# Kernel optimization log

Hardware: AMD Instinct MI355X
Metric: run time of the kernel (lower is better)

## Reference

```python
import jax, jax.numpy as jnp
import numpy as np

D = 128            # actual_dim
DM = 2 * D         # d_model = 256
DI = 2 * DM        # support-encoder inner dim = 512
H = 2 * DM         # LSTMCell hidden = 512
NUM_SYMBOLS = 200000
KNN_K = 10
PROCESS_STEPS = 4
BQ, BS, NN = 4096, 128, 64


def setup_inputs() -> dict:
    key = jax.random.key(0)
    ks = jax.random.split(key, 20)
    ri = lambda k, shape, hi: jax.random.randint(k, shape, 0, hi)
    rn = lambda k, shape, s=0.05: jax.random.normal(k, shape, jnp.float32) * s
    emb = rn(ks[0], (NUM_SYMBOLS + 1, D), 0.1).at[NUM_SYMBOLS].set(0.0)  # padding row
    return {
        "query": ri(ks[1], (BQ, 2), NUM_SYMBOLS),
        "support": ri(ks[2], (BS, 2), NUM_SYMBOLS),
        "q_l_conn": ri(ks[3], (BQ, NN, 2), NUM_SYMBOLS),
        "q_l_deg": ri(ks[4], (BQ,), NN),
        "q_r_conn": ri(ks[5], (BQ, NN, 2), NUM_SYMBOLS),
        "q_r_deg": ri(ks[6], (BQ,), NN),
        "s_l_conn": ri(ks[7], (BS, NN, 2), NUM_SYMBOLS),
        "s_l_deg": ri(ks[8], (BS,), NN),
        "s_r_conn": ri(ks[9], (BS, NN, 2), NUM_SYMBOLS),
        "s_r_deg": ri(ks[10], (BS,), NN),
        "emb": emb,
        "gcn_W": rn(ks[11], (D, 2 * D)),
        "gcn_wb": jnp.zeros((D,), jnp.float32),
        "gcn_b": jnp.zeros((D,), jnp.float32),
        "se_w1": rn(ks[12], (DI, DM)),
        "se_b1": jnp.zeros((DI,), jnp.float32),
        "se_w2": rn(ks[13], (DM, DI)),
        "se_b2": jnp.zeros((DM,), jnp.float32),
        "ln_g": jnp.ones((DM,), jnp.float32),
        "ln_b": jnp.zeros((DM,), jnp.float32),
        "W_ih": rn(ks[14], (4 * H, DM)),
        "W_hh": rn(ks[15], (4 * H, H)),
        "b_ih": jnp.zeros((4 * H,), jnp.float32),
        "b_hh": jnp.zeros((4 * H,), jnp.float32),
    }


def _cos(a, b, eps=1e-8):
    num = jnp.sum(a * b, -1)
    den = jnp.maximum(jnp.linalg.norm(a, axis=-1), eps) * jnp.maximum(jnp.linalg.norm(b, axis=-1), eps)
    return num / den


def _neighbor_encoder(emb, gcn_W, gcn_wb, gcn_b, conn, ent_ids):
    rel = emb[conn[..., 0]]                     # [B,N,D]
    ent = emb[conn[..., 1]]                     # [B,N,D]
    center = emb[ent_ids][:, None, :]           # [B,1,D]
    sim = _cos(center, ent)                     # [B,N]
    _, idx = jax.lax.top_k(sim, KNN_K)          # [B,K]
    rel_k = jnp.take_along_axis(rel, idx[..., None], axis=1)
    ent_k = jnp.take_along_axis(ent, idx[..., None], axis=1)
    cat = jnp.concatenate([rel_k, ent_k], -1)   # [B,K,2D]
    h = jnp.einsum('bkf,df->bkd', cat, gcn_W) + gcn_wb + gcn_b
    return jnp.tanh(h.mean(axis=1))             # [B,D]


def _support_encoder(x, w1, b1, w2, b2, g, b):
    # residual FFN + LayerNorm (GMatching SupportEncoder), dropout off (eval)
    out = jax.nn.relu(x @ w1.T + b1) @ w2.T + b2
    y = out + x
    mu = y.mean(-1, keepdims=True)
    var = ((y - mu) ** 2).mean(-1, keepdims=True)
    return (y - mu) / jnp.sqrt(var + 1e-5) * g + b


def _query_encoder(support, query, W_ih, W_hh, b_ih, b_hh):
    # GMatching attentive LSTM process block. support: [1,DM], query: [B,DM]
    B = query.shape[0]
    h_r = jnp.zeros((B, H), query.dtype)
    c = jnp.zeros((B, H), query.dtype)
    h = query
    for _ in range(PROCESS_STEPS):
        gates = query @ W_ih.T + b_ih + h_r @ W_hh.T + b_hh
        i, f, g_, o = jnp.split(gates, 4, axis=-1)  # torch LSTMCell gate order
        c = jax.nn.sigmoid(f) * c + jax.nn.sigmoid(i) * jnp.tanh(g_)
        h_new = jax.nn.sigmoid(o) * jnp.tanh(c)     # [B,H]
        h = query + h_new[:, :DM]                   # [B,DM]
        attn = jax.nn.softmax(h @ support.T, axis=1)  # [B,1]
        r = attn @ support                          # [B,DM]
        h_r = jnp.concatenate([h, r], axis=1)       # [B,H]
    return h


def reference(query, support, q_l_conn, q_l_deg, q_r_conn, q_r_deg,
              s_l_conn, s_l_deg, s_r_conn, s_r_deg,
              emb, gcn_W, gcn_wb, gcn_b,
              se_w1, se_b1, se_w2, se_b2, ln_g, ln_b,
              W_ih, W_hh, b_ih, b_hh):
    ne = lambda conn, ids: _neighbor_encoder(emb, gcn_W, gcn_wb, gcn_b, conn, ids)
    q_nb = jnp.concatenate([ne(q_l_conn, query[:, 0]), ne(q_r_conn, query[:, 1])], -1)    # [BQ,DM]
    s_nb = jnp.concatenate([ne(s_l_conn, support[:, 0]), ne(s_r_conn, support[:, 1])], -1)  # [BS,DM]
    se = lambda x: _support_encoder(x, se_w1, se_b1, se_w2, se_b2, ln_g, ln_b)
    support_g = se(s_nb).mean(axis=0, keepdims=True)  # [1,DM]
    query_g = se(q_nb)                                # [BQ,DM]
    qf = _query_encoder(support_g, query_g, W_ih, W_hh, b_ih, b_hh)
    l2 = lambda x: x / jnp.maximum(jnp.linalg.norm(x, axis=-1, keepdims=True), 1e-12)
    return (l2(qf) @ l2(support_g).T).squeeze(-1)     # [BQ]
```

## Files before the change

### kernel.cpp

```cpp
#include <hip/hip_runtime.h>
#include <hip/hip_bf16.h>

#define D   128
#define DM  256
#define DI  512
#define HH  512
#define KNN 10
#define NN  64
#define BQ  4096
#define BS  128
#define BM2 (BQ + BS)
#define G2  1024
#define GK  256
#define NSYM 200000

__device__ __forceinline__ float sigmoidf_(float x) {
    return 1.f / (1.f + __expf(-x));
}
__device__ __forceinline__ float tanh_fast(float x) {
    x = fminf(fmaxf(x, -20.f), 20.f);
    float e = __expf(2.f * x);
    return (e - 1.f) / (e + 1.f);
}
__device__ __forceinline__ ushort f2bf(float x) {
    union { float f; unsigned u; } v; v.f = x;
    unsigned r = (v.u + 0x7fffu + ((v.u >> 16) & 1u)) >> 16;
    return (ushort)r;
}

typedef __bf16  bf16x8  __attribute__((ext_vector_type(8)));
typedef float   floatx4 __attribute__((ext_vector_type(4)));

__global__ __launch_bounds__(256) void prep_kernel(
    const float* __restrict__ W_ih, const float* __restrict__ W_hh,
    const float* __restrict__ b_ih, const float* __restrict__ b_hh,
    const float* __restrict__ se_w1, const float* __restrict__ se_w2,
    ushort* __restrict__ wih_bf, ushort* __restrict__ whh_bf,
    float* __restrict__ bsumP, ushort* __restrict__ w1_bf,
    ushort* __restrict__ w2_bf)
{
    int bid = blockIdx.x;
    int tid = threadIdx.x;
    if (bid < G2) {
        int n = bid;
        int bn = n >> 7, r = n & 127;
        int half = (r >> 6) & 1, j = (r >> 4) & 3, l = r & 15;
        int u = bn * 32 + half * 16 + l;
        int oldrow = j * 512 + u;
        wih_bf[n * 256 + tid] = f2bf(W_ih[(size_t)oldrow * DM + tid]);
        whh_bf[n * 256 + tid] = f2bf(W_hh[(size_t)oldrow * HH + tid]);
        if (tid == 0) bsumP[n] = b_ih[oldrow] + b_hh[oldrow];
    } else {
        int idx = (bid - G2) * 256 + tid;
        w1_bf[idx] = f2bf(se_w1[idx]);
        w2_bf[idx] = f2bf(se_w2[idx]);
    }
}

__global__ __launch_bounds__(256) void ne_kernel(
    const int* __restrict__ q_l, const int* __restrict__ q_r,
    const int* __restrict__ q_ids,
    const int* __restrict__ s_l, const int* __restrict__ s_r,
    const int* __restrict__ s_ids,
    const float* __restrict__ emb,
    float* __restrict__ catm_out)
{
    int bid = blockIdx.x;
    const int *conn_l, *conn_r, *ids;
    int row;
    if (bid < BQ * 2) { conn_l = q_l; conn_r = q_r; ids = q_ids; row = bid >> 1; }
    else { conn_l = s_l; conn_r = s_r; ids = s_ids; row = (bid - BQ * 2) >> 1; }
    int side = bid & 1;
    const int* conn = (side ? conn_r : conn_l) + (size_t)row * NN * 2;
    int cid = ids[row * 2 + side];

    __shared__ int   connb[NN * 2];
    __shared__ float sim[NN];
    __shared__ int   selr[KNN], sele[KNN];

    int tid = threadIdx.x;
    int wave = tid >> 6, lane = tid & 63;
    int grp = lane >> 4, l16 = lane & 15;

    if (tid < NN * 2) connb[tid] = conn[tid];
    const float* cp = &emb[(size_t)cid * D + l16 * 8];
    float4 c4a = *(const float4*)cp;
    float4 c4b = *(const float4*)(cp + 4);
    float cs = c4a.x * c4a.x + c4a.y * c4a.y + c4a.z * c4a.z + c4a.w * c4a.w
             + c4b.x * c4b.x + c4b.y * c4b.y + c4b.z * c4b.z + c4b.w * c4b.w;
    #pragma unroll
    for (int off = 8; off; off >>= 1) cs += __shfl_xor(cs, off);
    float cnorm = fmaxf(sqrtf(cs), 1e-8f);
    __syncthreads();

    float4 ea[4], eb[4];
    #pragma unroll
    for (int b = 0; b < 4; b++) {
        int j = wave * 16 + b * 4 + grp;
        int eid = connb[j * 2 + 1];
        const float* ep = &emb[(size_t)eid * D + l16 * 8];
        ea[b] = *(const float4*)ep;
        eb[b] = *(const float4*)(ep + 4);
    }
    #pragma unroll
    for (int b = 0; b < 4; b++) {
        int j = wave * 16 + b * 4 + grp;
        float dot = c4a.x * ea[b].x + c4a.y * ea[b].y + c4a.z * ea[b].z + c4a.w * ea[b].w
                  + c4b.x * eb[b].x + c4b.y * eb[b].y + c4b.z * eb[b].z + c4b.w * eb[b].w;
        float ee  = ea[b].x * ea[b].x + ea[b].y * ea[b].y + ea[b].z * ea[b].z + ea[b].w * ea[b].w
                  + eb[b].x * eb[b].x + eb[b].y * eb[b].y + eb[b].z * eb[b].z + eb[b].w * eb[b].w;
        #pragma unroll
        for (int off = 8; off; off >>= 1) {
            dot += __shfl_xor(dot, off);
            ee  += __shfl_xor(ee, off);
        }
        if (l16 == 0) sim[j] = dot / (cnorm * fmaxf(sqrtf(ee), 1e-8f));
    }
    __syncthreads();

    if (wave == 0) {
        float s = sim[lane];
        int id = lane;
        for (int k = 0; k < KNN; k++) {
            float bs = s; int bi = id;
            #pragma unroll
            for (int off = 32; off; off >>= 1) {
                float os = __shfl_xor(bs, off);
                int   oi = __shfl_xor(bi, off);
                if (os > bs || (os == bs && oi < bi)) { bs = os; bi = oi; }
            }
            if (lane == 0) { selr[k] = connb[bi * 2]; sele[k] = connb[bi * 2 + 1]; }
            if (id == bi) s = -__builtin_inff();
        }
    }
    __syncthreads();

    float acc = 0.f;
    if (tid < D) {
        #pragma unroll
        for (int k = 0; k < KNN; k++) acc += emb[(size_t)selr[k] * D + tid];
    } else {
        int d = tid - D;
        #pragma unroll
        for (int k = 0; k < KNN; k++) acc += emb[(size_t)sele[k] * D + d];
    }
    catm_out[(size_t)bid * DM + tid] = acc * (1.f / KNN);
}

#define GR 16
__global__ __launch_bounds__(256) void gcn_kernel(
    const float* __restrict__ catm, const float* __restrict__ gcn_W,
    const float* __restrict__ gcn_wb, const float* __restrict__ gcn_b,
    float* __restrict__ out, ushort* __restrict__ out_bf)
{
    __shared__ float cs[GR][DM];
    __shared__ float pp[GR][DM];
    int tid = threadIdx.x;
    int m0 = blockIdx.x * GR;
    #pragma unroll
    for (int t = 0; t < 4; t++) {
        int chunk = tid + 256 * t;
        int r = chunk >> 6, c4 = chunk & 63;
        *(float4*)&cs[r][c4 * 4] = *(const float4*)&catm[(size_t)(m0 + r) * DM + c4 * 4];
    }
    __syncthreads();

    int d = tid & 127, half = tid >> 7;
    float a[GR];
    #pragma unroll
    for (int r = 0; r < GR; r++) a[r] = 0.f;
    const float4* W4 = (const float4*)(gcn_W + (size_t)d * DM + half * D);
    for (int f4 = 0; f4 < D / 4; ++f4) {
        float4 w = W4[f4];
        #pragma unroll
        for (int r = 0; r < GR; r++) {
            const float* c = &cs[r][half * D + f4 * 4];
            a[r] += w.x * c[0] + w.y * c[1] + w.z * c[2] + w.w * c[3];
        }
    }
    #pragma unroll
    for (int r = 0; r < GR; r++) pp[r][tid] = a[r];
    __syncthreads();
    if (tid < D) {
        #pragma unroll
        for (int r = 0; r < GR; r++) {
            float h = pp[r][tid] + pp[r][tid + D] + gcn_wb[tid] + gcn_b[tid];
            float th = tanh_fast(h);
            out[(size_t)(m0 + r) * D + tid] = th;
            out_bf[(size_t)(m0 + r) * D + tid] = f2bf(th);
        }
    }
}

#define BMT 128
#define BNT 128
#define BKT 64
#define LDP (BKT + 8)

#define GEMM_CORE(AP, BP, KDIM)                                               \
    floatx4 acc[4][4];                                                        \
    _Pragma("unroll")                                                         \
    for (int i = 0; i < 4; i++)                                               \
        _Pragma("unroll")                                                     \
        for (int j = 0; j < 4; j++) acc[i][j] = (floatx4){0.f, 0.f, 0.f, 0.f};\
    for (int k0 = 0; k0 < (KDIM); k0 += BKT) {                                \
        __syncthreads();                                                      \
        _Pragma("unroll")                                                     \
        for (int t = 0; t < 4; t++) {                                         \
            int chunk = tid + 256 * t;                                        \
            int r = chunk >> 3;                                               \
            int c8 = (chunk & 7) * 8;                                         \
            *(uint4*)&As[r][c8] = *(const uint4*)&(AP)[(size_t)(bm * BMT + r) * (KDIM) + k0 + c8]; \
            *(uint4*)&Bs[r][c8] = *(const uint4*)&(BP)[(size_t)(bn * BNT + r) * (KDIM) + k0 + c8]; \
        }                                                                     \
        __syncthreads();                                                      \
        _Pragma("unroll")                                                     \
        for (int kk = 0; kk < BKT; kk += 32) {                                \
            bf16x8 af[4], bf[4];                                              \
            _Pragma("unroll")                                                 \
            for (int i = 0; i < 4; i++)                                       \
                af[i] = *(const bf16x8*)&As[wm + i * 16 + l16][kk + quad * 8];\
            _Pragma("unroll")                                                 \
            for (int j = 0; j < 4; j++)                                       \
                bf[j] = *(const bf16x8*)&Bs[wn + j * 16 + l16][kk + quad * 8];\
            _Pragma("unroll")                                                 \
            for (int i = 0; i < 4; i++)                                       \
                _Pragma("unroll")                                             \
                for (int j = 0; j < 4; j++)                                   \
                    acc[i][j] = __builtin_amdgcn_mfma_f32_16x16x32_bf16(      \
                        af[i], bf[j], acc[i][j], 0, 0, 0);                    \
        }                                                                     \
    }

#define GEMM_PRE()                                                            \
    __shared__ __align__(16) ushort As[BMT][LDP];                             \
    __shared__ __align__(16) ushort Bs[BNT][LDP];                             \
    int tid = threadIdx.x;                                                    \
    int wave = tid >> 6, lane = tid & 63;                                     \
    int quad = lane >> 4, l16 = lane & 15;                                    \
    int bm = blockIdx.x, bn = blockIdx.y;                                     \
    int wm = (wave >> 1) * 64, wn = (wave & 1) * 64;                          \
    (void)wave;

__global__ __launch_bounds__(256) void se_gemm1_kernel(
    const ushort* __restrict__ A, const ushort* __restrict__ B,
    const float* __restrict__ b1, ushort* __restrict__ Cbf)
{
    GEMM_PRE();
    GEMM_CORE(A, B, DM);
    #pragma unroll
    for (int i = 0; i < 4; i++) {
        #pragma unroll
        for (int j = 0; j < 4; j++) {
            int row = bm * BMT + wm + i * 16 + quad * 4;
            int col = bn * BNT + wn + j * 16 + l16;
            float bb = b1[col];
            #pragma unroll
            for (int rr = 0; rr < 4; rr++)
                Cbf[(size_t)(row + rr) * DI + col] = f2bf(fmaxf(acc[i][j][rr] + bb, 0.f));
        }
    }
}

__global__ __launch_bounds__(256) void se_gemm2_kernel(
    const ushort* __restrict__ A, const ushort* __restrict__ B,
    const float* __restrict__ b2, const float* __restrict__ xres,
    float* __restrict__ C)
{
    GEMM_PRE();
    GEMM_CORE(A, B, DI);
    #pragma unroll
    for (int i = 0; i < 4; i++) {
        #pragma unroll
        for (int j = 0; j < 4; j++) {
            int row = bm * BMT + wm + i * 16 + quad * 4;
            int col = bn * BNT + wn + j * 16 + l16;
            float bb = b2[col];
            #pragma unroll
            for (int rr = 0; rr < 4; rr++)
                C[(size_t)(row + rr) * DM + col] =
                    acc[i][j][rr] + bb + xres[(size_t)(row + rr) * DM + col];
        }
    }
}

#define LN_ROWS 8
__global__ __launch_bounds__(256) void ln_kernel(
    const float* __restrict__ ys, const float* __restrict__ g,
    const float* __restrict__ b, float* __restrict__ outf,
    ushort* __restrict__ outbf)
{
    int tid = threadIdx.x;
    int wave = tid >> 6, lane = tid & 63;
    int r0 = blockIdx.x * LN_ROWS;
    for (int rr = 0; rr < 2; ++rr) {
        int r = r0 + wave * 2 + rr;
        float vals[4];
        float s = 0.f;
        #pragma unroll
        for (int e = 0; e < 4; e++) {
            vals[e] = ys[(size_t)r * DM + e * 64 + lane];
            s += vals[e];
        }
        #pragma unroll
        for (int off = 32; off; off >>= 1) s += __shfl_xor(s, off);
        float mu = s * (1.f / DM);
        float v = 0.f;
        #pragma unroll
        for (int e = 0; e < 4; e++) { float dd = vals[e] - mu; v += dd * dd; }
        #pragma unroll
        for (int off = 32; off; off >>= 1) v += __shfl_xor(v, off);
        float rstd = rsqrtf(v * (1.f / DM) + 1e-5f);
        #pragma unroll
        for (int e = 0; e < 4; e++) {
            int dd = e * 64 + lane;
            float ov = (vals[e] - mu) * rstd * g[dd] + b[dd];
            outf[(size_t)r * DM + dd] = ov;
            outbf[(size_t)r * DM + dd] = f2bf(ov);
        }
    }
}

__global__ __launch_bounds__(256) void sgw_kernel(
    const float* __restrict__ ln_f, const float* __restrict__ W_hh,
    const float* __restrict__ b_ih, const float* __restrict__ b_hh,
    float* __restrict__ sg, float* __restrict__ gaddP)
{
    __shared__ float s[DM];
    int tid = threadIdx.x;
    float a = 0.f;
    for (int r = 0; r < BS; r++) a += ln_f[(size_t)(BQ + r) * DM + tid];
    a *= (1.f / BS);
    s[tid] = a;
    if (blockIdx.x == 0) sg[tid] = a;
    __syncthreads();

    int idx = blockIdx.x * 256 + tid;
    int g = idx >> 8, u = idx & 255;
    int oldrow = g * 512 + u;
    const float4* w4 = (const float4*)(W_hh + (size_t)oldrow * HH + DM);
    float acc = 0.f;
    for (int f4 = 0; f4 < DM / 4; ++f4) {
        float4 w = w4[f4];
        acc += w.x * s[f4 * 4] + w.y * s[f4 * 4 + 1] + w.z * s[f4 * 4 + 2] + w.w * s[f4 * 4 + 3];
    }
    float bs = b_ih[oldrow] + b_hh[oldrow];
    int n = (u >> 5) * 128 + ((u >> 4) & 1) * 64 + g * 16 + (u & 15);
    gaddP[n] = bs + acc;
}

__global__ __launch_bounds__(256) void lstm_gemm0_kernel(
    const ushort* __restrict__ A, const ushort* __restrict__ B,
    const float* __restrict__ bsumP, const float* __restrict__ lnf,
    float* __restrict__ P0f, float* __restrict__ Cf, ushort* __restrict__ h_out)
{
    GEMM_PRE();
    GEMM_CORE(A, B, GK);
    int u = bn * 32 + (wn ? 16 : 0) + l16;
    size_t tile = (size_t)bm * 8 + bn;
    float b4[4];
    #pragma unroll
    for (int j = 0; j < 4; j++) b4[j] = bsumP[bn * 128 + wn + j * 16 + l16];
    #pragma unroll
    for (int i = 0; i < 4; i++) {
        int row = bm * BMT + wm + i * 16 + quad * 4;
        #pragma unroll
        for (int j = 0; j < 4; j++)
            *(floatx4*)&P0f[((tile * 16 + i * 4 + j) * 256 + tid) * 4] = acc[i][j];
        floatx4 cv4;
        #pragma unroll
        for (int rr = 0; rr < 4; rr++) {
            float iv = acc[i][0][rr] + b4[0];
            float gv = acc[i][2][rr] + b4[2];
            float ov = acc[i][3][rr] + b4[3];
            float cv = sigmoidf_(iv) * tanh_fast(gv);
            cv4[rr] = cv;
            float h = lnf[(size_t)(row + rr) * DM + u] + sigmoidf_(ov) * tanh_fast(cv);
            h_out[(size_t)(row + rr) * DM + u] = f2bf(h);
        }
        *(floatx4*)&Cf[((tile * 4 + i) * 256 + tid) * 4] = cv4;
    }
}

__global__ __launch_bounds__(256) void lstm_step_kernel(
    const ushort* __restrict__ A, const ushort* __restrict__ B,
    const float* __restrict__ P0f, const float* __restrict__ gaddP,
    const float* __restrict__ lnf, float* __restrict__ Cf,
    ushort* __restrict__ h_out, float* __restrict__ hf_out, int last)
{
    GEMM_PRE();
    GEMM_CORE(A, B, GK);
    int u = bn * 32 + (wn ? 16 : 0) + l16;
    size_t tile = (size_t)bm * 8 + bn;
    float g4[4];
    #pragma unroll
    for (int j = 0; j < 4; j++) g4[j] = gaddP[bn * 128 + wn + j * 16 + l16];
    #pragma unroll
    for (int i = 0; i < 4; i++) {
        int row = bm * BMT + wm + i * 16 + quad * 4;
        floatx4 p0[4];
        #pragma unroll
        for (int j = 0; j < 4; j++)
            p0[j] = *(const floatx4*)&P0f[((tile * 16 + i * 4 + j) * 256 + tid) * 4];
        floatx4 cprev = *(const floatx4*)&Cf[((tile * 4 + i) * 256 + tid) * 4];
        floatx4 cnew;
        #pragma unroll
        for (int rr = 0; rr < 4; rr++) {
            float iv = acc[i][0][rr] + p0[0][rr] + g4[0];
            float fv = acc[i][1][rr] + p0[1][rr] + g4[1];
            float gv = acc[i][2][rr] + p0[2][rr] + g4[2];
            float ov = acc[i][3][rr] + p0[3][rr] + g4[3];
            float cv = sigmoidf_(fv) * cprev[rr] + sigmoidf_(iv) * tanh_fast(gv);
            cnew[rr] = cv;
            float h = lnf[(size_t)(row + rr) * DM + u] + sigmoidf_(ov) * tanh_fast(cv);
            if (last) hf_out[(size_t)(row + rr) * DM + u] = h;
            else      h_out[(size_t)(row + rr) * DM + u] = f2bf(h);
        }
        *(floatx4*)&Cf[((tile * 4 + i) * 256 + tid) * 4] = cnew;
    }
}

__global__ __launch_bounds__(256) void final_kernel(
    const float* __restrict__ h_ws, const float* __restrict__ sg,
    float* __restrict__ outp)
{
    __shared__ float sgs[DM];
    int tid = threadIdx.x;
    sgs[tid] = sg[tid];
    __syncthreads();
    int wave = tid >> 6, lane = tid & 63;
    float sn = 0.f;
    #pragma unroll
    for (int e = 0; e < 4; e++) { float v = sgs[e * 64 + lane]; sn += v * v; }
    #pragma unroll
    for (int off = 32; off; off >>= 1) sn += __shfl_xor(sn, off);
    float sgnorm = fmaxf(sqrtf(sn), 1e-12f);

    int row = blockIdx.x * 4 + wave;
    const float* h = h_ws + (size_t)row * DM;
    float dot = 0.f, hn = 0.f;
    #pragma unroll
    for (int e = 0; e < 4; e++) {
        float hv = h[e * 64 + lane];
        dot += hv * sgs[e * 64 + lane];
        hn += hv * hv;
    }
    #pragma unroll
    for (int off = 32; off; off >>= 1) { dot += __shfl_xor(dot, off); hn += __shfl_xor(hn, off); }
    if (lane == 0) outp[row] = dot / (fmaxf(sqrtf(hn), 1e-12f) * sgnorm);
}

extern "C" void kernel_launch(void* const* d_in, const int* in_sizes, int n_in,
                              void* d_out, int out_size, void* d_ws, size_t ws_size,
                              hipStream_t stream)
{
    const int* query    = (const int*)d_in[0];
    const int* support  = (const int*)d_in[1];
    const int* q_l_conn = (const int*)d_in[2];
    const int* q_r_conn = (const int*)d_in[4];
    const int* s_l_conn = (const int*)d_in[6];
    const int* s_r_conn = (const int*)d_in[8];
    const float* emb    = (const float*)d_in[10];
    const float* gcn_W  = (const float*)d_in[11];
    const float* gcn_wb = (const float*)d_in[12];
    const float* gcn_b  = (const float*)d_in[13];
    const float* se_w1  = (const float*)d_in[14];
    const float* se_b1  = (const float*)d_in[15];
    const float* se_w2  = (const float*)d_in[16];
    const float* se_b2  = (const float*)d_in[17];
    const float* ln_g   = (const float*)d_in[18];
    const float* ln_b   = (const float*)d_in[19];
    const float* W_ih   = (const float*)d_in[20];
    const float* W_hh   = (const float*)d_in[21];
    const float* b_ih   = (const float*)d_in[22];
    const float* b_hh   = (const float*)d_in[23];
    float* out = (float*)d_out;

    char* wsb = (char*)d_ws;
    float*  xf     = (float*)wsb;  wsb += (size_t)BM2 * DM * 4;
    ushort* xb     = (ushort*)wsb; wsb += (size_t)BM2 * DM * 2;
    ushort* t1_bf  = (ushort*)wsb; wsb += (size_t)BM2 * DI * 2;
    float*  ys     = (float*)wsb;  wsb += (size_t)BM2 * DM * 4;
    float*  ln_f   = (float*)wsb;  wsb += (size_t)BM2 * DM * 4;
    ushort* ln_bf  = (ushort*)wsb; wsb += (size_t)BM2 * DM * 2;
    float*  sg     = (float*)wsb;  wsb += DM * 4;
    float*  bsumP  = (float*)wsb;  wsb += G2 * 4;
    float*  gaddP  = (float*)wsb;  wsb += G2 * 4;
    ushort* wih_bf = (ushort*)wsb; wsb += (size_t)G2 * DM * 2;
    ushort* whh_bf = (ushort*)wsb; wsb += (size_t)G2 * DM * 2;
    ushort* w1_bf  = (ushort*)wsb; wsb += (size_t)DI * DM * 2;
    ushort* w2_bf  = (ushort*)wsb; wsb += (size_t)DM * DI * 2;
    float*  P0f    = (float*)wsb;  wsb += (size_t)BQ * G2 * 4;
    float*  Cf     = (float*)wsb;  wsb += (size_t)BQ * DM * 4;
    ushort* h_bfA  = (ushort*)wsb; wsb += (size_t)BQ * DM * 2;
    ushort* h_bfB  = (ushort*)wsb; wsb += (size_t)BQ * DM * 2;
    float*  h_f    = (float*)wsb;  wsb += (size_t)BQ * DM * 4;

    float* catm = P0f;

    prep_kernel<<<G2 + 512, 256, 0, stream>>>(
        W_ih, W_hh, b_ih, b_hh, se_w1, se_w2,
        wih_bf, whh_bf, bsumP, w1_bf, w2_bf);
    ne_kernel<<<BQ * 2 + BS * 2, 256, 0, stream>>>(
        q_l_conn, q_r_conn, query, s_l_conn, s_r_conn, support,
        emb, catm);
    gcn_kernel<<<(BM2 * 2) / GR, 256, 0, stream>>>(catm, gcn_W, gcn_wb, gcn_b,
                                                   xf, xb);
    { dim3 g1(BM2 / BMT, DI / BNT);
      se_gemm1_kernel<<<g1, 256, 0, stream>>>(xb, w1_bf, se_b1, t1_bf); }
    { dim3 g2(BM2 / BMT, DM / BNT);
      se_gemm2_kernel<<<g2, 256, 0, stream>>>(t1_bf, w2_bf, se_b2, xf, ys); }
    ln_kernel<<<BM2 / LN_ROWS, 256, 0, stream>>>(ys, ln_g, ln_b, ln_f, ln_bf);
    sgw_kernel<<<G2 / 256, 256, 0, stream>>>(ln_f, W_hh, b_ih, b_hh, sg, gaddP);

    dim3 ggrid(BQ / BMT, G2 / BNT);
    lstm_gemm0_kernel<<<ggrid, 256, 0, stream>>>(ln_bf, wih_bf, bsumP, ln_f,
                                                 P0f, Cf, h_bfA);
    lstm_step_kernel<<<ggrid, 256, 0, stream>>>(h_bfA, whh_bf, P0f, gaddP, ln_f,
                                                Cf, h_bfB, h_f, 0);
    lstm_step_kernel<<<ggrid, 256, 0, stream>>>(h_bfB, whh_bf, P0f, gaddP, ln_f,
                                                Cf, h_bfA, h_f, 0);
    lstm_step_kernel<<<ggrid, 256, 0, stream>>>(h_bfA, whh_bf, P0f, gaddP, ln_f,
                                                Cf, h_bfB, h_f, 1);
    final_kernel<<<BQ / 4, 256, 0, stream>>>(h_f, sg, out);
}
```

Before: 376.2 us.

## Fuse LSTM steps into one persistent kernel with group barriers

Replaces the four separate LSTM GEMM launches with one persistent kernel of 256 blocks. Each block keeps its input-projection result, cell state and LN residual in registers, and keeps the W_hh tile resident in LDS. The eight blocks sharing a row tile synchronise between steps through atomic counter barriers. This removes the P0f and Cf round-trips through global memory, the repeated weight reloads and the launch overhead. The cost is a spin-wait barrier that assumes all 256 blocks are co-resident, plus heavy register and LDS use at one block per CU.

```diff
diff --git a/kernel.cpp b/kernel.cpp
--- a/kernel.cpp
+++ b/kernel.cpp
@@ -37,7 +37,7 @@
     const float* __restrict__ se_w1, const float* __restrict__ se_w2,
     ushort* __restrict__ wih_bf, ushort* __restrict__ whh_bf,
     float* __restrict__ bsumP, ushort* __restrict__ w1_bf,
-    ushort* __restrict__ w2_bf)
+    ushort* __restrict__ w2_bf, int* __restrict__ lbar)
 {
     int bid = blockIdx.x;
     int tid = threadIdx.x;
@@ -50,10 +50,12 @@
         wih_bf[n * 256 + tid] = f2bf(W_ih[(size_t)oldrow * DM + tid]);
         whh_bf[n * 256 + tid] = f2bf(W_hh[(size_t)oldrow * HH + tid]);
         if (tid == 0) bsumP[n] = b_ih[oldrow] + b_hh[oldrow];
-    } else {
+    } else if (bid < G2 + 512) {
         int idx = (bid - G2) * 256 + tid;
         w1_bf[idx] = f2bf(se_w1[idx]);
         w2_bf[idx] = f2bf(se_w2[idx]);
+    } else {
+        if (tid < 128) lbar[tid] = 0;
     }
 }
 
@@ -349,74 +351,152 @@
     gaddP[n] = bs + acc;
 }
 
-__global__ __launch_bounds__(256) void lstm_gemm0_kernel(
-    const ushort* __restrict__ A, const ushort* __restrict__ B,
-    const float* __restrict__ bsumP, const float* __restrict__ lnf,
-    float* __restrict__ P0f, float* __restrict__ Cf, ushort* __restrict__ h_out)
-{
-    GEMM_PRE();
-    GEMM_CORE(A, B, GK);
+#define SWZ(r, c16) (((c16) ^ ((r) & 7)) << 3)
+
+#define STAGE_TILE(DSTARR, SRCPTR, STRIDE)                                     \
+    _Pragma("unroll")                                                          \
+    for (int t = 0; t < 16; t++) {                                             \
+        int ch = t * 256 + tid;                                                \
+        int r = ch >> 5, c16 = ch & 31;                                        \
+        *(uint4*)&DSTARR[r][SWZ(r, c16)] =                                     \
+            *(const uint4*)&(SRCPTR)[(size_t)r * (STRIDE) + c16 * 8];          \
+    }
+
+#define LDS_GEMM(ACC)                                                          \
+    _Pragma("unroll")                                                          \
+    for (int kk = 0; kk < GK; kk += 32) {                                      \
+        bf16x8 af[4], bv[4];                                                   \
+        int c16 = (kk >> 3) + quad;                                            \
+        _Pragma("unroll")                                                      \
+        for (int i = 0; i < 4; i++) {                                          \
+            int rw = wm + i * 16 + l16;                                        \
+            af[i] = *(const bf16x8*)&AS[rw][SWZ(rw, c16)];                     \
+        }                                                                      \
+        _Pragma("unroll")                                                      \
+        for (int j = 0; j < 4; j++) {                                          \
+            int rw = wn + j * 16 + l16;                                        \
+            bv[j] = *(const bf16x8*)&WS[rw][SWZ(rw, c16)];                     \
+        }                                                                      \
+        _Pragma("unroll")                                                      \
+        for (int i = 0; i < 4; i++)                                            \
+            _Pragma("unroll")                                                  \
+            for (int j = 0; j < 4; j++)                                        \
+                ACC[i][j] = __builtin_amdgcn_mfma_f32_16x16x32_bf16(           \
+                    af[i], bv[j], ACC[i][j], 0, 0, 0);                         \
+    }
+
+__device__ __forceinline__ void group_barrier(int* cnt, int tid) {
+    __threadfence();
+    __syncthreads();
+    if (tid == 0) {
+        __hip_atomic_fetch_add(cnt, 1, __ATOMIC_RELEASE, __HIP_MEMORY_SCOPE_AGENT);
+        while (__hip_atomic_load(cnt, __ATOMIC_ACQUIRE, __HIP_MEMORY_SCOPE_AGENT) < 8) {}
+    }
+    __syncthreads();
+    __threadfence();
+}
+
+__global__ __launch_bounds__(256, 1) void lstm_fused_kernel(
+    const ushort* __restrict__ lnbf,
+    const ushort* __restrict__ wihP,
+    const ushort* __restrict__ whhP,
+    const float* __restrict__ bsumP,
+    const float* __restrict__ gaddP,
+    const float* __restrict__ lnf,
+    ushort* __restrict__ hA,
+    ushort* __restrict__ hB,
+    float* __restrict__ hF,
+    int* __restrict__ lbar)
+{
+    __shared__ __align__(16) ushort AS[128][256];
+    __shared__ __align__(16) ushort WS[128][256];
+
+    int tid = threadIdx.x;
+    int wave = tid >> 6, lane = tid & 63;
+    int quad = lane >> 4, l16 = lane & 15;
+    int bid = blockIdx.x;
+    int bm = bid >> 3, bn = bid & 7;
+    int wm = (wave >> 1) * 64, wn = (wave & 1) * 64;
     int u = bn * 32 + (wn ? 16 : 0) + l16;
-    size_t tile = (size_t)bm * 8 + bn;
-    float b4[4];
-    #pragma unroll
-    for (int j = 0; j < 4; j++) b4[j] = bsumP[bn * 128 + wn + j * 16 + l16];
+    int* mybar = lbar + bm * 4;
+
+    STAGE_TILE(WS, wihP + (size_t)(bn * 128) * GK, GK);
+    STAGE_TILE(AS, lnbf + (size_t)(bm * 128) * GK, GK);
+
+    float b4[4], g4[4];
+    #pragma unroll
+    for (int j = 0; j < 4; j++) {
+        b4[j] = bsumP[bn * 128 + wn + j * 16 + l16];
+        g4[j] = gaddP[bn * 128 + wn + j * 16 + l16];
+    }
+    float lnb[4][4];
     #pragma unroll
     for (int i = 0; i < 4; i++) {
-        int row = bm * BMT + wm + i * 16 + quad * 4;
-        #pragma unroll
-        for (int j = 0; j < 4; j++)
-            *(floatx4*)&P0f[((tile * 16 + i * 4 + j) * 256 + tid) * 4] = acc[i][j];
-        floatx4 cv4;
+        int row = bm * 128 + wm + i * 16 + quad * 4;
+        #pragma unroll
+        for (int rr = 0; rr < 4; rr++)
+            lnb[i][rr] = lnf[(size_t)(row + rr) * DM + u];
+    }
+    __syncthreads();
+
+    floatx4 p0[4][4];
+    #pragma unroll
+    for (int i = 0; i < 4; i++)
+        #pragma unroll
+        for (int j = 0; j < 4; j++) p0[i][j] = (floatx4){0.f, 0.f, 0.f, 0.f};
+    LDS_GEMM(p0);
+
+    float cf_[4][4];
+    #pragma unroll
+    for (int i = 0; i < 4; i++) {
+        int row = bm * 128 + wm + i * 16 + quad * 4;
         #pragma unroll
         for (int rr = 0; rr < 4; rr++) {
-            float iv = acc[i][0][rr] + b4[0];
-            float gv = acc[i][2][rr] + b4[2];
-            float ov = acc[i][3][rr] + b4[3];
+            float iv = p0[i][0][rr] + b4[0];
+            float gv = p0[i][2][rr] + b4[2];
+            float ov = p0[i][3][rr] + b4[3];
             float cv = sigmoidf_(iv) * tanh_fast(gv);
-            cv4[rr] = cv;
-            float h = lnf[(size_t)(row + rr) * DM + u] + sigmoidf_(ov) * tanh_fast(cv);
-            h_out[(size_t)(row + rr) * DM + u] = f2bf(h);
-        }
-        *(floatx4*)&Cf[((tile * 4 + i) * 256 + tid) * 4] = cv4;
-    }
-}
-
-__global__ __launch_bounds__(256) void lstm_step_kernel(
-    const ushort* __restrict__ A, const ushort* __restrict__ B,
-    const float* __restrict__ P0f, const float* __restrict__ gaddP,
-    const float* __restrict__ lnf, float* __restrict__ Cf,
-    ushort* __restrict__ h_out, float* __restrict__ hf_out, int last)
-{
-    GEMM_PRE();
-    GEMM_CORE(A, B, GK);
-    int u = bn * 32 + (wn ? 16 : 0) + l16;
-    size_t tile = (size_t)bm * 8 + bn;
-    float g4[4];
-    #pragma unroll
-    for (int j = 0; j < 4; j++) g4[j] = gaddP[bn * 128 + wn + j * 16 + l16];
-    #pragma unroll
-    for (int i = 0; i < 4; i++) {
-        int row = bm * BMT + wm + i * 16 + quad * 4;
-        floatx4 p0[4];
-        #pragma unroll
-        for (int j = 0; j < 4; j++)
-            p0[j] = *(const floatx4*)&P0f[((tile * 16 + i * 4 + j) * 256 + tid) * 4];
-        floatx4 cprev = *(const floatx4*)&Cf[((tile * 4 + i) * 256 + tid) * 4];
-        floatx4 cnew;
-        #pragma unroll
-        for (int rr = 0; rr < 4; rr++) {
-            float iv = acc[i][0][rr] + p0[0][rr] + g4[0];
-            float fv = acc[i][1][rr] + p0[1][rr] + g4[1];
-            float gv = acc[i][2][rr] + p0[2][rr] + g4[2];
-            float ov = acc[i][3][rr] + p0[3][rr] + g4[3];
-            float cv = sigmoidf_(fv) * cprev[rr] + sigmoidf_(iv) * tanh_fast(gv);
-            cnew[rr] = cv;
-            float h = lnf[(size_t)(row + rr) * DM + u] + sigmoidf_(ov) * tanh_fast(cv);
-            if (last) hf_out[(size_t)(row + rr) * DM + u] = h;
-            else      h_out[(size_t)(row + rr) * DM + u] = f2bf(h);
-        }
-        *(floatx4*)&Cf[((tile * 4 + i) * 256 + tid) * 4] = cnew;
+            cf_[i][rr] = cv;
+            float h = lnb[i][rr] + sigmoidf_(ov) * tanh_fast(cv);
+            hA[(size_t)(row + rr) * DM + u] = f2bf(h);
+        }
+    }
+    __syncthreads();
+    STAGE_TILE(WS, whhP + (size_t)(bn * 128) * GK, GK);
+    group_barrier(mybar + 0, tid);
+
+    const ushort* hin = hA;
+    ushort* hout = hB;
+    #pragma unroll 1
+    for (int step = 2; step <= 4; ++step) {
+        STAGE_TILE(AS, hin + (size_t)(bm * 128) * DM, DM);
+        __syncthreads();
+        floatx4 acc[4][4];
+        #pragma unroll
+        for (int i = 0; i < 4; i++)
+            #pragma unroll
+            for (int j = 0; j < 4; j++) acc[i][j] = (floatx4){0.f, 0.f, 0.f, 0.f};
+        LDS_GEMM(acc);
+        #pragma unroll
+        for (int i = 0; i < 4; i++) {
+            int row = bm * 128 + wm + i * 16 + quad * 4;
+            #pragma unroll
+            for (int rr = 0; rr < 4; rr++) {
+                float iv = acc[i][0][rr] + p0[i][0][rr] + g4[0];
+                float fv = acc[i][1][rr] + p0[i][1][rr] + g4[1];
+                float gv = acc[i][2][rr] + p0[i][2][rr] + g4[2];
+                float ov = acc[i][3][rr] + p0[i][3][rr] + g4[3];
+                float cv = sigmoidf_(fv) * cf_[i][rr] + sigmoidf_(iv) * tanh_fast(gv);
+                cf_[i][rr] = cv;
+                float h = lnb[i][rr] + sigmoidf_(ov) * tanh_fast(cv);
+                if (step == 4) hF[(size_t)(row + rr) * DM + u] = h;
+                else           hout[(size_t)(row + rr) * DM + u] = f2bf(h);
+            }
+        }
+        if (step < 4) {
+            group_barrier(mybar + (step - 1), tid);
+            const ushort* t = hin; hin = hout; hout = (ushort*)t;
+        }
     }
 }
 
@@ -486,21 +566,19 @@
     float*  sg     = (float*)wsb;  wsb += DM * 4;
     float*  bsumP  = (float*)wsb;  wsb += G2 * 4;
     float*  gaddP  = (float*)wsb;  wsb += G2 * 4;
+    int*    lbar   = (int*)wsb;    wsb += 128 * 4;
     ushort* wih_bf = (ushort*)wsb; wsb += (size_t)G2 * DM * 2;
     ushort* whh_bf = (ushort*)wsb; wsb += (size_t)G2 * DM * 2;
     ushort* w1_bf  = (ushort*)wsb; wsb += (size_t)DI * DM * 2;
     ushort* w2_bf  = (ushort*)wsb; wsb += (size_t)DM * DI * 2;
-    float*  P0f    = (float*)wsb;  wsb += (size_t)BQ * G2 * 4;
-    float*  Cf     = (float*)wsb;  wsb += (size_t)BQ * DM * 4;
+    float*  catm   = (float*)wsb;  wsb += (size_t)(BM2 * 2) * DM * 4;
     ushort* h_bfA  = (ushort*)wsb; wsb += (size_t)BQ * DM * 2;
     ushort* h_bfB  = (ushort*)wsb; wsb += (size_t)BQ * DM * 2;
     float*  h_f    = (float*)wsb;  wsb += (size_t)BQ * DM * 4;
 
-    float* catm = P0f;
-
-    prep_kernel<<<G2 + 512, 256, 0, stream>>>(
+    prep_kernel<<<G2 + 512 + 1, 256, 0, stream>>>(
         W_ih, W_hh, b_ih, b_hh, se_w1, se_w2,
-        wih_bf, whh_bf, bsumP, w1_bf, w2_bf);
+        wih_bf, whh_bf, bsumP, w1_bf, w2_bf, lbar);
     ne_kernel<<<BQ * 2 + BS * 2, 256, 0, stream>>>(
         q_l_conn, q_r_conn, query, s_l_conn, s_r_conn, support,
         emb, catm);
@@ -513,14 +591,7 @@
     ln_kernel<<<BM2 / LN_ROWS, 256, 0, stream>>>(ys, ln_g, ln_b, ln_f, ln_bf);
     sgw_kernel<<<G2 / 256, 256, 0, stream>>>(ln_f, W_hh, b_ih, b_hh, sg, gaddP);
 
-    dim3 ggrid(BQ / BMT, G2 / BNT);
-    lstm_gemm0_kernel<<<ggrid, 256, 0, stream>>>(ln_bf, wih_bf, bsumP, ln_f,
-                                                 P0f, Cf, h_bfA);
-    lstm_step_kernel<<<ggrid, 256, 0, stream>>>(h_bfA, whh_bf, P0f, gaddP, ln_f,
-                                                Cf, h_bfB, h_f, 0);
-    lstm_step_kernel<<<ggrid, 256, 0, stream>>>(h_bfB, whh_bf, P0f, gaddP, ln_f,
-                                                Cf, h_bfA, h_f, 0);
-    lstm_step_kernel<<<ggrid, 256, 0, stream>>>(h_bfA, whh_bf, P0f, gaddP, ln_f,
-                                                Cf, h_bfB, h_f, 1);
+    lstm_fused_kernel<<<256, 256, 0, stream>>>(
+        ln_bf, wih_bf, whh_bf, bsumP, gaddP, ln_f, h_bfA, h_bfB, h_f, lbar);
     final_kernel<<<BQ / 4, 256, 0, stream>>>(h_f, sg, out);
 }
```

New measurement: 464.0 us. +23.3%, slower.
